# Optimization experiments

Hardware: AMD Instinct MI355X
Metric: run time of the kernel (lower is better)

The kernel has to match this reference:

```python
import jax, jax.numpy as jnp
import numpy as np
from jax import lax

B, S, H, D, NH, L, NC = 64, 512, 64, 128, 8, 4, 5
DT = 0.01

def _xavier(key, shape, gain=0.1):
    a = gain * np.sqrt(6.0 / (shape[0] + shape[1]))
    return jax.random.uniform(key, shape, jnp.float32, -a, a)

def setup_inputs():
    key = jax.random.key(0)
    ks = jax.random.split(key, 20)
    # strictly increasing positive times with spacing exactly dt -> one Euler step per interval
    times = (jnp.arange(S, dtype=jnp.float32) + 1.0) * DT
    feats = jax.random.uniform(ks[0], (B, S, 2), jnp.float32, 0.5, 5.0)
    time_series = jnp.concatenate([jnp.broadcast_to(times[None, :, None], (B, S, 1)), feats], axis=2)
    mask = jnp.ones((B, S), dtype=bool)
    noise = jax.random.normal(ks[1], (S - 1, B, H), jnp.float32)  # standard normal; scaled by sqrt(dt) inside
    n = lambda k, sh: 0.02 * jax.random.normal(k, sh, jnp.float32)
    return dict(
        time_series=time_series, mask=mask, noise=noise,
        dW1=_xavier(ks[2], (H + 1, 2 * H)), db1=jnp.zeros(2 * H, jnp.float32),
        dW2=_xavier(ks[3], (2 * H, H)), db2=jnp.zeros(H, jnp.float32),
        dW3=_xavier(ks[4], (H, H)), db3=jnp.zeros(H, jnp.float32),
        gW1=_xavier(ks[5], (H + 1, 2 * H)), gb1=jnp.zeros(2 * H, jnp.float32),
        gW2=_xavier(ks[6], (2 * H, H)), gb2=jnp.zeros(H, jnp.float32),
        min_diffusion=jnp.float32(0.05), max_drift=jnp.float32(1.0),
        in_W=n(ks[7], (H, D)), in_b=jnp.zeros(D, jnp.float32),
        Wq=n(ks[8], (L, D, D)), bq=jnp.zeros((L, D), jnp.float32),
        Wk=n(ks[9], (L, D, D)), bk=jnp.zeros((L, D), jnp.float32),
        Wv=n(ks[10], (L, D, D)), bv=jnp.zeros((L, D), jnp.float32),
        Wo=n(ks[11], (L, D, D)), bo=jnp.zeros((L, D), jnp.float32),
        ln1_s=jnp.ones((L, D), jnp.float32), ln1_b=jnp.zeros((L, D), jnp.float32),
        fW1=n(ks[12], (L, D, 4 * D)), fb1=jnp.zeros((L, 4 * D), jnp.float32),
        fW2=n(ks[13], (L, 4 * D, D)), fb2=jnp.zeros((L, D), jnp.float32),
        ln2_s=jnp.ones((L, D), jnp.float32), ln2_b=jnp.zeros((L, D), jnp.float32),
        cW1=n(ks[14], (D, D // 2)), cb1=jnp.zeros(D // 2, jnp.float32),
        cW2=n(ks[15], (D // 2, NC)), cb2=jnp.zeros(NC, jnp.float32),
    )

def _ln(x, s, b):
    m = x.mean(-1, keepdims=True)
    v = ((x - m) ** 2).mean(-1, keepdims=True)
    return (x - m) * lax.rsqrt(v + 1e-5) * s + b

def reference(time_series, mask, noise, dW1, db1, dW2, db2, dW3, db3,
              gW1, gb1, gW2, gb2, min_diffusion, max_drift,
              in_W, in_b, Wq, bq, Wk, bk, Wv, bv, Wo, bo,
              ln1_s, ln1_b, fW1, fb1, fW2, fb2, ln2_s, ln2_b,
              cW1, cb1, cW2, cb2):
    b, s = time_series.shape[:2]
    h = dW3.shape[1]
    nin = min(3, h)  # min(input_dim, hidden_channels)
    times = time_series[:, :, 0]

    # initial SDE state
    y0 = jnp.full((b, h), 0.1, time_series.dtype)
    y0 = y0.at[:, :nin].set(jnp.clip(time_series[:, 0, :nin], 0.01, 10.0))

    # per-interval left times, step sizes, Brownian increments (batch-shared time, element 0)
    ts0 = times[0]                        # (S,)
    t_left = ts0[:-1]                     # (S-1,)
    hstep = ts0[1:] - ts0[:-1]            # (S-1,)
    dW = noise * jnp.sqrt(hstep)[:, None, None]  # (S-1, B, H)

    def euler_step(y, inp):
        t, hh, dw = inp
        t_col = jnp.broadcast_to(jnp.reshape(t, (1, 1)), (y.shape[0], 1))
        ty = jnp.concatenate([y, t_col], axis=1)              # (B, H+1)
        # drift coeff net: Linear-Tanh-Linear-Tanh-Linear, clamped
        dc = jnp.tanh(ty @ dW1 + db1)
        dc = jnp.tanh(dc @ dW2 + db2)
        dc = dc @ dW3 + db3
        dc = jnp.clip(dc, -jnp.abs(max_drift), jnp.abs(max_drift))
        f = dc * y
        # diffusion coeff net: Linear-Tanh-Linear-Softplus + |min_diffusion|
        gc = jnp.tanh(ty @ gW1 + gb1)
        gc = jax.nn.softplus(gc @ gW2 + gb2) + jnp.abs(min_diffusion)
        g = gc * jnp.clip(y, -10.0, 10.0)
        y1 = jnp.clip(y + f * hh + g * dw, 0.01, 10.0)  # Euler-Maruyama + post-solve clamp
        return y1, y1

    _, traj = lax.scan(euler_step, y0, (t_left, hstep, dW))   # (S-1, B, H)
    sde_features = jnp.concatenate([y0[None], traj], axis=0).transpose(1, 0, 2)  # (B, S, H)
    mf = mask[..., None].astype(sde_features.dtype)
    sde_features = sde_features * mf

    # ContiFormer (standard post-LN transformer encoder over SDE features)
    x = sde_features @ in_W + in_b                            # (B, S, D)
    d = x.shape[-1]
    dh = d // NH
    scale = 1.0 / np.sqrt(dh)
    neg = jnp.asarray(-1e9, x.dtype)
    for l in range(Wq.shape[0]):
        q = (x @ Wq[l] + bq[l]).reshape(b, s, NH, dh)
        k = (x @ Wk[l] + bk[l]).reshape(b, s, NH, dh)
        v = (x @ Wv[l] + bv[l]).reshape(b, s, NH, dh)
        scores = jnp.einsum('bqhd,bkhd->bhqk', q, k) * scale
        scores = jnp.where(mask[:, None, None, :], scores, neg)
        attn = jax.nn.softmax(scores, axis=-1)
        o = jnp.einsum('bhqk,bkhd->bqhd', attn, v).reshape(b, s, d) @ Wo[l] + bo[l]
        x = _ln(x + o, ln1_s[l], ln1_b[l])
        ff = jax.nn.relu(x @ fW1[l] + fb1[l]) @ fW2[l] + fb2[l]
        x = _ln(x + ff, ln2_s[l], ln2_b[l])

    pooled = (x * mf).sum(1) / jnp.maximum(mf.sum(1), 1.0)    # masked mean pool (B, D)
    logits = jax.nn.relu(pooled @ cW1 + cb1) @ cW2 + cb2      # (B, NC)
    return (logits, sde_features)
```

## Files before the change

kernel.cpp:

```cpp
#include <hip/hip_runtime.h>
#include <hip/hip_bf16.h>
#include <math.h>

#define BB 64
#define SS 512
#define HH 64
#define DD 128
#define NHD 8
#define ROWS (BB*SS)

typedef unsigned short u16;
typedef __attribute__((ext_vector_type(8))) short bf16x8;
typedef __attribute__((ext_vector_type(4))) float f32x4;

__device__ __forceinline__ u16 f2b(float f) {
  union { float f; unsigned u; } x; x.f = f;
  unsigned r = x.u + 0x7fffu + ((x.u >> 16) & 1u);
  return (u16)(r >> 16);
}

__device__ __forceinline__ float b2f(u16 u) {
  return __uint_as_float(((unsigned)u) << 16);
}

__device__ __forceinline__ unsigned cvt_pk_bf16(float lo, float hi) {
  unsigned r;
  asm("v_cvt_pk_bf16_f32 %0, %1, %2" : "=v"(r) : "v"(lo), "v"(hi));
  return r;
}

__device__ __forceinline__ float fast_tanh(float x) {
  float ax = fminf(fabsf(x), 15.f);
  float e = __expf(2.f * ax);
  float r = 1.f - __fdividef(2.f, e + 1.f);
  return copysignf(r, x);
}

__device__ __forceinline__ void barrier_lds() {
  __builtin_amdgcn_s_waitcnt(0xC07F);
  __builtin_amdgcn_s_barrier();
}

__device__ __forceinline__ float dpp_xor1_add(float x) {
  int pi = __float_as_int(x);
  int po = __builtin_amdgcn_update_dpp(0, pi, 0xB1 ,
                                       0xF, 0xF, true);
  return x + __int_as_float(po);
}

template <int CTRL>
__device__ __forceinline__ float dpp_add(float x) {
  int po = __builtin_amdgcn_update_dpp(0, __float_as_int(x), CTRL, 0xF, 0xF, true);
  return x + __int_as_float(po);
}
__device__ __forceinline__ float red16(float x) {
  x = dpp_add<0xB1>(x);
  x = dpp_add<0x4E>(x);
  x = dpp_add<0x141>(x);
  x = dpp_add<0x140>(x);
  return x;
}

__global__ __attribute__((amdgpu_flat_work_group_size(512, 512)))
__attribute__((amdgpu_waves_per_eu(2, 2))) void sde_kernel(
    const float* __restrict__ ts, const float* __restrict__ noise,
    const float* __restrict__ dW1, const float* __restrict__ db1,
    const float* __restrict__ dW2, const float* __restrict__ db2,
    const float* __restrict__ dW3, const float* __restrict__ db3,
    const float* __restrict__ gW1, const float* __restrict__ gb1,
    const float* __restrict__ gW2, const float* __restrict__ gb2,
    const float* __restrict__ pmind, const float* __restrict__ pmaxd,
    float* __restrict__ out, u16* __restrict__ outB) {
  const int b = blockIdx.x, t = threadIdx.x;
  const int w = t >> 6, lane = t & 63;
  const int drift = (w < 4) ? 1 : 0;
  const int wseg = w & 3;

  __shared__ float y_s[8][64];
  __shared__ float h1seg[8][32];
  __shared__ float h2c[8][64];
  __shared__ float pd[2][4][64];
  __shared__ float pg[2][4][64];
  __shared__ float tl_s[512], hs_s[512], sq_s[512];

  const float mind = fabsf(pmind[0]);
  const float maxd = fabsf(pmaxd[0]);

  const int colA = wseg * 32 + (lane >> 1);
  const int hA = lane & 1;
  const float* W1 = drift ? dW1 : gW1;
  float wA[32];
#pragma unroll
  for (int k = 0; k < 32; k++) wA[k] = W1[(hA * 32 + k) * 128 + colA];
  const float wAt = W1[64 * 128 + colA];
  const float bA = (drift ? db1 : gb1)[colA];

  const float* W2 = drift ? dW2 : gW2;
  float wB[32];
#pragma unroll
  for (int k = 0; k < 32; k++) wB[k] = W2[(wseg * 32 + k) * 64 + lane];
  const float bBd = db2[lane], bBg = gb2[lane];

  float wC[64];
#pragma unroll
  for (int k = 0; k < 64; k++) wC[k] = dW3[k * 64 + lane];
  const float bC = db3[lane];

  tl_s[t & 511] = ts[(t & 511) * 3];
  __syncthreads();
  if (t < 511) {
    float hh = tl_s[t + 1] - tl_s[t];
    hs_s[t] = hh;
    sq_s[t] = sqrtf(hh);
  }

  float ymine = 0.1f;
  if (lane < 3) ymine = fminf(fmaxf(ts[b * 1536 + lane], 0.01f), 10.f);
  y_s[w][lane] = ymine;
  if (w == 0) out[(long)b * 32768 + lane] = ymine;
  if (w == 1) outB[((long)b * 512) * 64 + lane] = f2b(ymine);

  const long nofs = (long)b * 64 + lane;
  float nz0 = noise[nofs];
  float nz1 = noise[4096 + nofs];
  float nz2 = noise[2 * 4096 + nofs];
  float nz3 = noise[3 * 4096 + nofs];
  __syncthreads();

  for (int i = 0; i < 511; i++) {
    const int buf = i & 1;
    const float tl = tl_s[i];
    const float hh = hs_s[i];
    const float sq = sq_s[i];

    const float nz = nz0;
    nz0 = nz1; nz1 = nz2; nz2 = nz3;
    if (i + 4 < 511) nz3 = noise[(long)(i + 4) * 4096 + nofs];

    float a0 = 0.f, a1 = 0.f, a2 = 0.f, a3 = 0.f;
#pragma unroll
    for (int g = 0; g < 8; g++) {
      float4 yv = *(const float4*)&y_s[w][hA * 32 + g * 4];
      a0 += yv.x * wA[g * 4 + 0];
      a1 += yv.y * wA[g * 4 + 1];
      a2 += yv.z * wA[g * 4 + 2];
      a3 += yv.w * wA[g * 4 + 3];
    }
    float p1 = (a0 + a1) + (a2 + a3);
    p1 += hA ? (tl * wAt) : bA;
    p1 = dpp_xor1_add(p1);
    float h1v = fast_tanh(p1);
    if (hA == 0) h1seg[w][lane >> 1] = h1v;

    float c0 = 0.f, c1 = 0.f, c2 = 0.f, c3 = 0.f;
#pragma unroll
    for (int g = 0; g < 8; g++) {
      float4 hv = *(const float4*)&h1seg[w][g * 4];
      c0 += hv.x * wB[g * 4 + 0];
      c1 += hv.y * wB[g * 4 + 1];
      c2 += hv.z * wB[g * 4 + 2];
      c3 += hv.w * wB[g * 4 + 3];
    }
    float psum = (c0 + c1) + (c2 + c3);
    if (drift) pd[buf][wseg][lane] = psum;
    else       pg[buf][wseg][lane] = psum;

    barrier_lds();

    float sd = ((pd[buf][0][lane] + pd[buf][1][lane]) +
                (pd[buf][2][lane] + pd[buf][3][lane])) + bBd;
    float h2v = fast_tanh(sd);
    float sg = ((pg[buf][0][lane] + pg[buf][1][lane]) +
                (pg[buf][2][lane] + pg[buf][3][lane])) + bBg;
    float gc = fmaxf(sg, 0.f) + __logf(1.f + __expf(-fabsf(sg))) + mind;
    h2c[w][lane] = h2v;

    float d0 = 0.f, d1 = 0.f, d2 = 0.f, d3 = 0.f;
#pragma unroll
    for (int g = 0; g < 16; g++) {
      float4 hv = *(const float4*)&h2c[w][g * 4];
      d0 += hv.x * wC[g * 4 + 0];
      d1 += hv.y * wC[g * 4 + 1];
      d2 += hv.z * wC[g * 4 + 2];
      d3 += hv.w * wC[g * 4 + 3];
    }
    float dc = fminf(fmaxf((d0 + d1) + (d2 + d3) + bC, -maxd), maxd);

    float yo = ymine;
    float yn = yo + dc * yo * hh + gc * fminf(fmaxf(yo, -10.f), 10.f) * nz * sq;
    yn = fminf(fmaxf(yn, 0.01f), 10.f);
    y_s[w][lane] = yn;
    ymine = yn;
    if (w == 0) out[(long)b * 32768 + (i + 1) * 64 + lane] = yn;
    if (w == 1) outB[((long)b * 512 + i + 1) * 64 + lane] = f2b(yn);
  }
}

__global__ __launch_bounds__(256) void prep_weights(
    const float* __restrict__ in_W, const float* __restrict__ Wq,
    const float* __restrict__ Wk, const float* __restrict__ Wv,
    const float* __restrict__ Wo, const float* __restrict__ fW1,
    const float* __restrict__ fW2,
    u16* __restrict__ inWt, u16* __restrict__ qkvWt, u16* __restrict__ Wot,
    u16* __restrict__ fW1t, u16* __restrict__ fW2t) {
  const int z = blockIdx.z, layer = blockIdx.y, tile = blockIdx.x;
  const float* src; u16* dst; int R, C, nl;
  switch (z) {
    case 0: src = in_W; dst = inWt; R = 64; C = 128; nl = 1; break;
    case 1: src = Wq + layer * 16384; dst = qkvWt + layer * 49152; R = 128; C = 128; nl = 4; break;
    case 2: src = Wk + layer * 16384; dst = qkvWt + layer * 49152 + 16384; R = 128; C = 128; nl = 4; break;
    case 3: src = Wv + layer * 16384; dst = qkvWt + layer * 49152 + 32768; R = 128; C = 128; nl = 4; break;
    case 4: src = Wo + layer * 16384; dst = Wot + layer * 16384; R = 128; C = 128; nl = 4; break;
    case 5: src = fW1 + layer * 65536; dst = fW1t + layer * 65536; R = 128; C = 512; nl = 4; break;
    default: src = fW2 + layer * 65536; dst = fW2t + layer * 65536; R = 512; C = 128; nl = 4; break;
  }
  const int nt = (R / 32) * (C / 32);
  if (layer >= nl || tile >= nt) return;
  const int tpr = C / 32;
  const int r0 = (tile / tpr) * 32, c0 = (tile % tpr) * 32;
  __shared__ float tl[32][33];
  const int tx = threadIdx.x & 31, ty = threadIdx.x >> 5;
#pragma unroll
  for (int p = 0; p < 4; p++)
    tl[ty + 8 * p][tx] = src[(long)(r0 + ty + 8 * p) * C + c0 + tx];
  __syncthreads();
#pragma unroll
  for (int p = 0; p < 4; p++)
    dst[(long)(c0 + ty + 8 * p) * R + r0 + tx] = f2b(tl[tx][ty + 8 * p]);
}

__global__ __launch_bounds__(256) void mfma_gemm(
    const u16* __restrict__ A, const u16* __restrict__ Bt,
    const float* __restrict__ bias, u16* __restrict__ outB, int K, int N) {
  __shared__ u16 As[128 * 40];
  __shared__ u16 Bs[64 * 40];
  const int t = threadIdx.x;
  const int nb = blockIdx.x * 64;
  const long mb = (long)blockIdx.y * 128;
  const int lane = t & 63, wave = t >> 6;
  const int wm = (wave >> 1) * 64, wn = (wave & 1) * 32;
  const int fr = lane & 15, quad = lane >> 4;

  f32x4 zero = {0.f, 0.f, 0.f, 0.f};
  f32x4 acc[4][2];
#pragma unroll
  for (int mi = 0; mi < 4; mi++)
#pragma unroll
    for (int ni = 0; ni < 2; ni++) acc[mi][ni] = zero;

  for (int k0 = 0; k0 < K; k0 += 32) {
#pragma unroll
    for (int p = 0; p < 2; p++) {
      int idx = t + p * 256, row = idx >> 2, seg = idx & 3;
      int4 v = *(const int4*)&A[(mb + row) * K + k0 + seg * 8];
      *(int4*)&As[row * 40 + seg * 8] = v;
    }
    {
      int row = t >> 2, seg = t & 3;
      int4 v = *(const int4*)&Bt[(long)(nb + row) * K + k0 + seg * 8];
      *(int4*)&Bs[row * 40 + seg * 8] = v;
    }
    __syncthreads();
    bf16x8 af[4], bfr[2];
#pragma unroll
    for (int mi = 0; mi < 4; mi++)
      af[mi] = *(const bf16x8*)&As[(wm + mi * 16 + fr) * 40 + quad * 8];
#pragma unroll
    for (int ni = 0; ni < 2; ni++)
      bfr[ni] = *(const bf16x8*)&Bs[(wn + ni * 16 + fr) * 40 + quad * 8];
#pragma unroll
    for (int mi = 0; mi < 4; mi++)
#pragma unroll
      for (int ni = 0; ni < 2; ni++)
        acc[mi][ni] = __builtin_amdgcn_mfma_f32_16x16x32_bf16(
            af[mi], bfr[ni], acc[mi][ni], 0, 0, 0);
    __syncthreads();
  }

#pragma unroll
  for (int mi = 0; mi < 4; mi++)
#pragma unroll
    for (int ni = 0; ni < 2; ni++) {
      int col = nb + wn + ni * 16 + fr;
      float bv = bias[col];
#pragma unroll
      for (int r = 0; r < 4; r++) {
        long row = mb + wm + mi * 16 + quad * 4 + r;
        outB[row * N + col] = f2b(acc[mi][ni][r] + bv);
      }
    }
}

__global__ __launch_bounds__(512, 1) void layer_tail(
    const u16* __restrict__ ob, const u16* __restrict__ Wot,
    const float* __restrict__ bo, const float* __restrict__ ln1s,
    const float* __restrict__ ln1b, const u16* __restrict__ W1t,
    const float* __restrict__ fb1, const u16* __restrict__ W2t,
    const float* __restrict__ fb2, const float* __restrict__ ln2s,
    const float* __restrict__ ln2b, u16* __restrict__ xb) {
  __shared__ u16 As[64 * 136];
  __shared__ u16 Hs[64 * 520];
  __shared__ float s1[64][8], s2[64][8];
  __shared__ float mst[64][2];
  const int t = threadIdx.x;
  const long mb = (long)blockIdx.x * 64;
  const int w = t >> 6, lane = t & 63;
  const int fr = lane & 15, quad = lane >> 4;
  const int col = w * 16 + fr;
  const f32x4 z4 = {0.f, 0.f, 0.f, 0.f};

#pragma unroll
  for (int p = 0; p < 2; p++) {
    int c = t + p * 512;
    int row = c >> 4, sub = c & 15;
    *(int4*)&As[row * 136 + sub * 8] =
        *(const int4*)&ob[(mb + row) * DD + sub * 8];
  }
  __syncthreads();

  bf16x8 af[4][4];
#pragma unroll
  for (int m = 0; m < 4; m++)
#pragma unroll
    for (int c = 0; c < 4; c++)
      af[m][c] = *(const bf16x8*)&As[(m * 16 + fr) * 136 + c * 32 + quad * 8];

  f32x4 acc[4] = {z4, z4, z4, z4};
#pragma unroll
  for (int kc = 0; kc < 4; kc++) {
    bf16x8 bfr = *(const bf16x8*)&Wot[col * 128 + kc * 32 + quad * 8];
#pragma unroll
    for (int m = 0; m < 4; m++)
      acc[m] = __builtin_amdgcn_mfma_f32_16x16x32_bf16(af[m][kc], bfr,
                                                       acc[m], 0, 0, 0);
  }

  const float bov = bo[col], g1 = ln1s[col], be1 = ln1b[col];
  float vv[4][4];
#pragma unroll
  for (int m = 0; m < 4; m++)
#pragma unroll
    for (int r = 0; r < 4; r++) {
      int row = m * 16 + quad * 4 + r;
      float v = acc[m][r] + bov + b2f(xb[(mb + row) * DD + col]);
      vv[m][r] = v;
      float s = red16(v);
      float ss = red16(v * v);
      if (fr == 0) { s1[row][w] = s; s2[row][w] = ss; }
    }
  __syncthreads();
  {
    int row = lane;
    float4 a = *(const float4*)&s1[row][0];
    float4 bq4 = *(const float4*)&s1[row][4];
    float sumv = ((a.x + a.y) + (a.z + a.w)) +
                 ((bq4.x + bq4.y) + (bq4.z + bq4.w));
    float4 cq = *(const float4*)&s2[row][0];
    float4 dq = *(const float4*)&s2[row][4];
    float sumsq = ((cq.x + cq.y) + (cq.z + cq.w)) +
                  ((dq.x + dq.y) + (dq.z + dq.w));
    float mean = sumv * (1.f / 128.f);
    float var = sumsq * (1.f / 128.f) - mean * mean;
    mst[row][0] = mean;
    mst[row][1] = rsqrtf(var + 1e-5f);
  }
  __syncthreads();

  float xr[4][4];
#pragma unroll
  for (int m = 0; m < 4; m++)
#pragma unroll
    for (int r = 0; r < 4; r++) {
      int row = m * 16 + quad * 4 + r;
      float xv = (vv[m][r] - mst[row][0]) * mst[row][1] * g1 + be1;
      xr[m][r] = xv;
      As[row * 136 + col] = f2b(xv);
    }
  __syncthreads();

  bf16x8 af2[4][4];
#pragma unroll
  for (int m = 0; m < 4; m++)
#pragma unroll
    for (int c = 0; c < 4; c++)
      af2[m][c] = *(const bf16x8*)&As[(m * 16 + fr) * 136 + c * 32 + quad * 8];

#pragma unroll
  for (int nn = 0; nn < 4; nn++) {
    const int nt = w * 4 + nn;
    bf16x8 bfr[4];
#pragma unroll
    for (int c = 0; c < 4; c++)
      bfr[c] = *(const bf16x8*)&W1t[(nt * 16 + fr) * 128 + c * 32 + quad * 8];
    f32x4 a1[4] = {z4, z4, z4, z4};
#pragma unroll
    for (int c = 0; c < 4; c++)
#pragma unroll
      for (int m = 0; m < 4; m++)
        a1[m] = __builtin_amdgcn_mfma_f32_16x16x32_bf16(af2[m][c], bfr[c],
                                                        a1[m], 0, 0, 0);
    const float bv = fb1[nt * 16 + fr];
#pragma unroll
    for (int m = 0; m < 4; m++)
#pragma unroll
      for (int r = 0; r < 4; r++)
        Hs[(m * 16 + quad * 4 + r) * 520 + nt * 16 + fr] =
            f2b(fmaxf(a1[m][r] + bv, 0.f));
  }
  __syncthreads();

  f32x4 acc2[4] = {z4, z4, z4, z4};
#pragma unroll
  for (int kc = 0; kc < 16; kc++) {
    bf16x8 bfr2 = *(const bf16x8*)&W2t[col * 512 + kc * 32 + quad * 8];
    bf16x8 a2[4];
#pragma unroll
    for (int m = 0; m < 4; m++)
      a2[m] = *(const bf16x8*)&Hs[(m * 16 + fr) * 520 + kc * 32 + quad * 8];
#pragma unroll
    for (int m = 0; m < 4; m++)
      acc2[m] = __builtin_amdgcn_mfma_f32_16x16x32_bf16(a2[m], bfr2,
                                                        acc2[m], 0, 0, 0);
  }

  const float bv2 = fb2[col], g2 = ln2s[col], be2 = ln2b[col];
#pragma unroll
  for (int m = 0; m < 4; m++)
#pragma unroll
    for (int r = 0; r < 4; r++) {
      int row = m * 16 + quad * 4 + r;
      float v = acc2[m][r] + bv2 + xr[m][r];
      vv[m][r] = v;
      float s = red16(v);
      float ss = red16(v * v);
      if (fr == 0) { s1[row][w] = s; s2[row][w] = ss; }
    }
  __syncthreads();
  {
    int row = lane;
    float4 a = *(const float4*)&s1[row][0];
    float4 bq4 = *(const float4*)&s1[row][4];
    float sumv = ((a.x + a.y) + (a.z + a.w)) +
                 ((bq4.x + bq4.y) + (bq4.z + bq4.w));
    float4 cq = *(const float4*)&s2[row][0];
    float4 dq = *(const float4*)&s2[row][4];
    float sumsq = ((cq.x + cq.y) + (cq.z + cq.w)) +
                  ((dq.x + dq.y) + (dq.z + dq.w));
    float mean = sumv * (1.f / 128.f);
    float var = sumsq * (1.f / 128.f) - mean * mean;
    mst[row][0] = mean;
    mst[row][1] = rsqrtf(var + 1e-5f);
  }
  __syncthreads();

#pragma unroll
  for (int m = 0; m < 4; m++)
#pragma unroll
    for (int r = 0; r < 4; r++) {
      int row = m * 16 + quad * 4 + r;
      xb[(mb + row) * DD + col] =
          f2b((vv[m][r] - mst[row][0]) * mst[row][1] * g2 + be2);
    }
}

__global__ __launch_bounds__(256, 2) void qkv_attn(
    const u16* __restrict__ xb, const u16* __restrict__ qkvW,
    const float* __restrict__ bq, const float* __restrict__ bk,
    const float* __restrict__ bv, u16* __restrict__ Og) {
  const int bh = blockIdx.x;
  const int b = bh >> 3, h = bh & 7;
  __shared__ u16 Ks[512 * 24];
  __shared__ u16 Vt[16 * 520];
  __shared__ u16 Qs[512 * 24];
  const int t = threadIdx.x;
  const int w = t >> 6, lane = t & 63;
  const int fr = lane & 15, quad = lane >> 4;
  const long obase = ((long)b * SS) * DD + h * 16;
  const u16* xrow = xb + (long)b * SS * DD;

  const u16* Wq_h = qkvW + (h * 16) * 128;
  const u16* Wk_h = qkvW + 16384 + (h * 16) * 128;
  const u16* Wv_h = qkvW + 32768 + (h * 16) * 128;
  bf16x8 wqf[4], wkf[4], wvf[4];
#pragma unroll
  for (int c = 0; c < 4; c++) {
    wqf[c] = *(const bf16x8*)&Wq_h[fr * 128 + c * 32 + quad * 8];
    wkf[c] = *(const bf16x8*)&Wk_h[fr * 128 + c * 32 + quad * 8];
    wvf[c] = *(const bf16x8*)&Wv_h[fr * 128 + c * 32 + quad * 8];
  }
  const float bqv = bq[h * 16 + fr];
  const float bkv = bk[h * 16 + fr];
  const float bvv = bv[h * 16 + fr];
  const f32x4 z4 = {0.f, 0.f, 0.f, 0.f};
  const float qscale = 0.25f * 1.4426950408889634f;

  for (int tile = w; tile < 32; tile += 4) {
    const int t0 = tile * 16;
    bf16x8 af[4];
#pragma unroll
    for (int c = 0; c < 4; c++)
      af[c] = *(const bf16x8*)&xrow[(t0 + fr) * 128 + c * 32 + quad * 8];
    f32x4 qa = z4, ka = z4, va = z4;
#pragma unroll
    for (int c = 0; c < 4; c++) {
      qa = __builtin_amdgcn_mfma_f32_16x16x32_bf16(af[c], wqf[c], qa, 0, 0, 0);
      ka = __builtin_amdgcn_mfma_f32_16x16x32_bf16(af[c], wkf[c], ka, 0, 0, 0);
      va = __builtin_amdgcn_mfma_f32_16x16x32_bf16(af[c], wvf[c], va, 0, 0, 0);
    }
#pragma unroll
    for (int r = 0; r < 4; r++) {
      int row = t0 + quad * 4 + r;
      Qs[row * 24 + fr] = f2b((qa[r] + bqv) * qscale);
      Ks[row * 24 + fr] = f2b(ka[r] + bkv);
    }
    {
      const int t0q = t0 + quad * 4;
      const int r40 = t0q & 31;
      const int vbase = (t0q & ~31) + ((r40 & 12) << 1) + ((r40 & 16) >> 2);
      uint2 vvv;
      vvv.x = cvt_pk_bf16(va[0] + bvv, va[1] + bvv);
      vvv.y = cvt_pk_bf16(va[2] + bvv, va[3] + bvv);
      *(uint2*)&Vt[fr * 520 + vbase] = vvv;
    }
  }
  __syncthreads();

  for (int qt = w; qt < 32; qt += 4) {
    const int q0 = qt * 16;
    bf16x8 qf = {0, 0, 0, 0, 0, 0, 0, 0};
    if (quad < 2)
      qf = *(const bf16x8*)&Qs[(q0 + fr) * 24 + quad * 8];
    f32x4 oacc = {0.f, 0.f, 0.f, 0.f};
    float rsacc = 0.f;

    for (int kt = 0; kt < 16; kt++) {
      const int k0 = kt * 32;
      bf16x8 kf0 = {0, 0, 0, 0, 0, 0, 0, 0};
      bf16x8 kf1 = {0, 0, 0, 0, 0, 0, 0, 0};
      if (quad < 2) {
        kf0 = *(const bf16x8*)&Ks[(k0 + fr) * 24 + quad * 8];
        kf1 = *(const bf16x8*)&Ks[(k0 + 16 + fr) * 24 + quad * 8];
      }
      f32x4 slo = __builtin_amdgcn_mfma_f32_16x16x32_bf16(kf0, qf, z4, 0, 0, 0);
      f32x4 shi = __builtin_amdgcn_mfma_f32_16x16x32_bf16(kf1, qf, z4, 0, 0, 0);
      float p[8];
#pragma unroll
      for (int r = 0; r < 4; r++) {
        p[r] = __builtin_amdgcn_exp2f(slo[r]);
        p[4 + r] = __builtin_amdgcn_exp2f(shi[r]);
      }
      rsacc += ((p[0] + p[1]) + (p[2] + p[3])) +
               ((p[4] + p[5]) + (p[6] + p[7]));

      union { unsigned i[4]; bf16x8 v; } pu;
      pu.i[0] = cvt_pk_bf16(p[0], p[1]);
      pu.i[1] = cvt_pk_bf16(p[2], p[3]);
      pu.i[2] = cvt_pk_bf16(p[4], p[5]);
      pu.i[3] = cvt_pk_bf16(p[6], p[7]);
      bf16x8 vf = *(const bf16x8*)&Vt[fr * 520 + k0 + quad * 8];
      oacc = __builtin_amdgcn_mfma_f32_16x16x32_bf16(vf, pu.v, oacc, 0, 0, 0);
    }

    float lrun = rsacc;
    lrun += __shfl_xor(lrun, 16);
    lrun += __shfl_xor(lrun, 32);
    float inv = __fdividef(1.f, lrun);
    uint2 o;
    o.x = cvt_pk_bf16(oacc[0] * inv, oacc[1] * inv);
    o.y = cvt_pk_bf16(oacc[2] * inv, oacc[3] * inv);
    *(uint2*)&Og[obase + (long)(q0 + fr) * DD + quad * 4] = o;
  }
}

__global__ __launch_bounds__(512) void pool_kernel(const u16* __restrict__ X,
                                                   float* __restrict__ P) {
  const int b = blockIdx.x, t = threadIdx.x;
  const int c = t & 127, sg = t >> 7;
  __shared__ float red[4][128];
  float acc = 0.f;
  for (int s = sg; s < SS; s += 4)
    acc += b2f(X[((long)b * SS + s) * DD + c]);
  red[sg][c] = acc;
  __syncthreads();
  if (t < 128)
    P[b * DD + t] =
        (red[0][t] + red[1][t] + red[2][t] + red[3][t]) * (1.f / 512.f);
}

__global__ __launch_bounds__(64) void cls_kernel(
    const float* __restrict__ P, const float* __restrict__ W1,
    const float* __restrict__ b1, const float* __restrict__ W2,
    const float* __restrict__ b2, float* __restrict__ L) {
  const int b = blockIdx.x, t = threadIdx.x;
  __shared__ float sp[128];
  __shared__ float sh[64];
  sp[t] = P[b * DD + t];
  sp[t + 64] = P[b * DD + 64 + t];
  __syncthreads();
  float acc = b1[t];
  for (int k = 0; k < 128; k++) acc += sp[k] * W1[k * 64 + t];
  sh[t] = fmaxf(acc, 0.f);
  __syncthreads();
  if (t < 5) {
    float acc2 = b2[t];
    for (int k = 0; k < 64; k++) acc2 += sh[k] * W2[k * 5 + t];
    L[b * 5 + t] = acc2;
  }
}

extern "C" void kernel_launch(void* const* d_in, const int* in_sizes, int n_in,
                              void* d_out, int out_size, void* d_ws, size_t ws_size,
                              hipStream_t stream) {
  const float* ts    = (const float*)d_in[0];
  const float* noise = (const float*)d_in[2];
  const float* dW1   = (const float*)d_in[3];
  const float* db1   = (const float*)d_in[4];
  const float* dW2   = (const float*)d_in[5];
  const float* db2   = (const float*)d_in[6];
  const float* dW3   = (const float*)d_in[7];
  const float* db3   = (const float*)d_in[8];
  const float* gW1   = (const float*)d_in[9];
  const float* gb1   = (const float*)d_in[10];
  const float* gW2   = (const float*)d_in[11];
  const float* gb2   = (const float*)d_in[12];
  const float* mind  = (const float*)d_in[13];
  const float* maxd  = (const float*)d_in[14];
  const float* in_W  = (const float*)d_in[15];
  const float* in_b  = (const float*)d_in[16];
  const float* Wq    = (const float*)d_in[17];
  const float* bq    = (const float*)d_in[18];
  const float* Wk    = (const float*)d_in[19];
  const float* bk    = (const float*)d_in[20];
  const float* Wv    = (const float*)d_in[21];
  const float* bv    = (const float*)d_in[22];
  const float* Wo    = (const float*)d_in[23];
  const float* bo    = (const float*)d_in[24];
  const float* ln1s  = (const float*)d_in[25];
  const float* ln1b  = (const float*)d_in[26];
  const float* fW1   = (const float*)d_in[27];
  const float* fb1   = (const float*)d_in[28];
  const float* fW2   = (const float*)d_in[29];
  const float* fb2   = (const float*)d_in[30];
  const float* ln2s  = (const float*)d_in[31];
  const float* ln2b  = (const float*)d_in[32];
  const float* cW1   = (const float*)d_in[33];
  const float* cb1   = (const float*)d_in[34];
  const float* cW2   = (const float*)d_in[35];
  const float* cb2   = (const float*)d_in[36];

  float* logits = (float*)d_out;
  float* sde    = logits + BB * 5;

  char* W = (char*)d_ws;
  u16*  bxb    = (u16*)(W);
  u16*  bob    = (u16*)(W + (40u << 20));
  u16*  bsb    = (u16*)(W + (48u << 20));
  u16*  wts    = (u16*)(W + (52u << 20));
  float* bp    = (float*)(W + (54u << 20));

  u16* inWt  = wts;
  u16* qkvWt = inWt + 8192;
  u16* Wot   = qkvWt + 196608;
  u16* fW1t  = Wot + 65536;
  u16* fW2t  = fW1t + 262144;

  prep_weights<<<dim3(64, 4, 7), 256, 0, stream>>>(in_W, Wq, Wk, Wv, Wo, fW1, fW2,
                                                   inWt, qkvWt, Wot, fW1t, fW2t);

  sde_kernel<<<64, 512, 0, stream>>>(ts, noise, dW1, db1, dW2, db2, dW3, db3,
                                     gW1, gb1, gW2, gb2, mind, maxd, sde, bsb);

  mfma_gemm<<<dim3(2, 256), 256, 0, stream>>>(bsb, inWt, in_b, bxb, 64, 128);

  for (int l = 0; l < 4; l++) {
    qkv_attn<<<BB * NHD, 256, 0, stream>>>(bxb, qkvWt + l * 49152,
                                           bq + l * DD, bk + l * DD, bv + l * DD,
                                           bob);
    layer_tail<<<512, 512, 0, stream>>>(bob, Wot + l * 16384, bo + l * DD,
                                        ln1s + l * DD, ln1b + l * DD,
                                        fW1t + l * 65536, fb1 + l * 512,
                                        fW2t + l * 65536, fb2 + l * DD,
                                        ln2s + l * DD, ln2b + l * DD, bxb);
  }

  pool_kernel<<<BB, 512, 0, stream>>>(bxb, bp);
  cls_kernel<<<BB, 64, 0, stream>>>(bp, cW1, cb1, cW2, cb2, logits);
}
```

Before: 1.049 ms.

## Cut LDS and register use in layer_tail and qkv_attn to raise occupancy

```diff
diff --git a/kernel.cpp b/kernel.cpp
--- a/kernel.cpp
+++ b/kernel.cpp
@@ -39,6 +39,10 @@
 __device__ __forceinline__ void barrier_lds() {
   __builtin_amdgcn_s_waitcnt(0xC07F);
   __builtin_amdgcn_s_barrier();
+}
+
+__device__ __forceinline__ void wait_lds() {
+  __builtin_amdgcn_s_waitcnt(0xC07F);
 }
 
 __device__ __forceinline__ float dpp_xor1_add(float x) {
@@ -291,7 +295,7 @@
     }
 }
 
-__global__ __launch_bounds__(512, 1) void layer_tail(
+__global__ __launch_bounds__(512, 4) void layer_tail(
     const u16* __restrict__ ob, const u16* __restrict__ Wot,
     const float* __restrict__ bo, const float* __restrict__ ln1s,
     const float* __restrict__ ln1b, const u16* __restrict__ W1t,
@@ -299,7 +303,7 @@
     const float* __restrict__ fb2, const float* __restrict__ ln2s,
     const float* __restrict__ ln2b, u16* __restrict__ xb) {
   __shared__ u16 As[64 * 136];
-  __shared__ u16 Hs[64 * 520];
+  __shared__ u16 Hs[64 * 264];
   __shared__ float s1[64][8], s2[64][8];
   __shared__ float mst[64][2];
   const int t = threadIdx.x;
@@ -318,21 +322,15 @@
   }
   __syncthreads();
 
-  bf16x8 af[4][4];
-#pragma unroll
-  for (int m = 0; m < 4; m++)
-#pragma unroll
-    for (int c = 0; c < 4; c++)
-      af[m][c] = *(const bf16x8*)&As[(m * 16 + fr) * 136 + c * 32 + quad * 8];
-
   f32x4 acc[4] = {z4, z4, z4, z4};
 #pragma unroll
   for (int kc = 0; kc < 4; kc++) {
     bf16x8 bfr = *(const bf16x8*)&Wot[col * 128 + kc * 32 + quad * 8];
 #pragma unroll
-    for (int m = 0; m < 4; m++)
-      acc[m] = __builtin_amdgcn_mfma_f32_16x16x32_bf16(af[m][kc], bfr,
-                                                       acc[m], 0, 0, 0);
+    for (int m = 0; m < 4; m++) {
+      bf16x8 a = *(const bf16x8*)&As[(m * 16 + fr) * 136 + kc * 32 + quad * 8];
+      acc[m] = __builtin_amdgcn_mfma_f32_16x16x32_bf16(a, bfr, acc[m], 0, 0, 0);
+    }
   }
 
   const float bov = bo[col], g1 = ln1s[col], be1 = ln1b[col];
@@ -378,49 +376,48 @@
     }
   __syncthreads();
 
-  bf16x8 af2[4][4];
-#pragma unroll
-  for (int m = 0; m < 4; m++)
-#pragma unroll
-    for (int c = 0; c < 4; c++)
-      af2[m][c] = *(const bf16x8*)&As[(m * 16 + fr) * 136 + c * 32 + quad * 8];
-
-#pragma unroll
-  for (int nn = 0; nn < 4; nn++) {
-    const int nt = w * 4 + nn;
-    bf16x8 bfr[4];
-#pragma unroll
-    for (int c = 0; c < 4; c++)
-      bfr[c] = *(const bf16x8*)&W1t[(nt * 16 + fr) * 128 + c * 32 + quad * 8];
-    f32x4 a1[4] = {z4, z4, z4, z4};
-#pragma unroll
-    for (int c = 0; c < 4; c++)
+  f32x4 acc2[4] = {z4, z4, z4, z4};
+#pragma unroll
+  for (int c = 0; c < 2; c++) {
+    if (c) __syncthreads();
+#pragma unroll
+    for (int nn = 0; nn < 2; nn++) {
+      const int ntl = w * 2 + nn;
+      const int ntg = c * 16 + ntl;
+      f32x4 a1[4] = {z4, z4, z4, z4};
+#pragma unroll
+      for (int cc = 0; cc < 4; cc++) {
+        bf16x8 bfr =
+            *(const bf16x8*)&W1t[(ntg * 16 + fr) * 128 + cc * 32 + quad * 8];
+#pragma unroll
+        for (int m = 0; m < 4; m++) {
+          bf16x8 a =
+              *(const bf16x8*)&As[(m * 16 + fr) * 136 + cc * 32 + quad * 8];
+          a1[m] =
+              __builtin_amdgcn_mfma_f32_16x16x32_bf16(a, bfr, a1[m], 0, 0, 0);
+        }
+      }
+      const float bv = fb1[ntg * 16 + fr];
 #pragma unroll
       for (int m = 0; m < 4; m++)
-        a1[m] = __builtin_amdgcn_mfma_f32_16x16x32_bf16(af2[m][c], bfr[c],
-                                                        a1[m], 0, 0, 0);
-    const float bv = fb1[nt * 16 + fr];
-#pragma unroll
-    for (int m = 0; m < 4; m++)
-#pragma unroll
-      for (int r = 0; r < 4; r++)
-        Hs[(m * 16 + quad * 4 + r) * 520 + nt * 16 + fr] =
-            f2b(fmaxf(a1[m][r] + bv, 0.f));
-  }
-  __syncthreads();
-
-  f32x4 acc2[4] = {z4, z4, z4, z4};
-#pragma unroll
-  for (int kc = 0; kc < 16; kc++) {
-    bf16x8 bfr2 = *(const bf16x8*)&W2t[col * 512 + kc * 32 + quad * 8];
-    bf16x8 a2[4];
-#pragma unroll
-    for (int m = 0; m < 4; m++)
-      a2[m] = *(const bf16x8*)&Hs[(m * 16 + fr) * 520 + kc * 32 + quad * 8];
-#pragma unroll
-    for (int m = 0; m < 4; m++)
-      acc2[m] = __builtin_amdgcn_mfma_f32_16x16x32_bf16(a2[m], bfr2,
-                                                        acc2[m], 0, 0, 0);
+#pragma unroll
+        for (int r = 0; r < 4; r++)
+          Hs[(m * 16 + quad * 4 + r) * 264 + ntl * 16 + fr] =
+              f2b(fmaxf(a1[m][r] + bv, 0.f));
+    }
+    __syncthreads();
+#pragma unroll
+    for (int kc = 0; kc < 8; kc++) {
+      bf16x8 bfr2 =
+          *(const bf16x8*)&W2t[col * 512 + c * 256 + kc * 32 + quad * 8];
+#pragma unroll
+      for (int m = 0; m < 4; m++) {
+        bf16x8 a2 =
+            *(const bf16x8*)&Hs[(m * 16 + fr) * 264 + kc * 32 + quad * 8];
+        acc2[m] = __builtin_amdgcn_mfma_f32_16x16x32_bf16(a2, bfr2,
+                                                          acc2[m], 0, 0, 0);
+      }
+    }
   }
 
   const float bv2 = fb2[col], g2 = ln2s[col], be2 = ln2b[col];
@@ -463,7 +460,7 @@
     }
 }
 
-__global__ __launch_bounds__(256, 2) void qkv_attn(
+__global__ __launch_bounds__(256, 3) void qkv_attn(
     const u16* __restrict__ xb, const u16* __restrict__ qkvW,
     const float* __restrict__ bq, const float* __restrict__ bk,
     const float* __restrict__ bv, u16* __restrict__ Og) {
@@ -471,7 +468,7 @@
   const int b = bh >> 3, h = bh & 7;
   __shared__ u16 Ks[512 * 24];
   __shared__ u16 Vt[16 * 520];
-  __shared__ u16 Qs[512 * 24];
+  __shared__ u16 Qsc[4][16 * 24];
   const int t = threadIdx.x;
   const int w = t >> 6, lane = t & 63;
   const int fr = lane & 15, quad = lane >> 4;
@@ -494,8 +491,10 @@
   const f32x4 z4 = {0.f, 0.f, 0.f, 0.f};
   const float qscale = 0.25f * 1.4426950408889634f;
 
-  for (int tile = w; tile < 32; tile += 4) {
-    const int t0 = tile * 16;
+  bf16x8 qreg[8];
+#pragma unroll
+  for (int ti = 0; ti < 8; ti++) {
+    const int t0 = (w + ti * 4) * 16;
     bf16x8 af[4];
 #pragma unroll
     for (int c = 0; c < 4; c++)
@@ -510,8 +509,8 @@
 #pragma unroll
     for (int r = 0; r < 4; r++) {
       int row = t0 + quad * 4 + r;
-      Qs[row * 24 + fr] = f2b((qa[r] + bqv) * qscale);
       Ks[row * 24 + fr] = f2b(ka[r] + bkv);
+      Qsc[w][(quad * 4 + r) * 24 + fr] = f2b((qa[r] + bqv) * qscale);
     }
     {
       const int t0q = t0 + quad * 4;
@@ -522,14 +521,18 @@
       vvv.y = cvt_pk_bf16(va[2] + bvv, va[3] + bvv);
       *(uint2*)&Vt[fr * 520 + vbase] = vvv;
     }
-  }
-  __syncthreads();
-
-  for (int qt = w; qt < 32; qt += 4) {
-    const int q0 = qt * 16;
+    wait_lds();
     bf16x8 qf = {0, 0, 0, 0, 0, 0, 0, 0};
     if (quad < 2)
-      qf = *(const bf16x8*)&Qs[(q0 + fr) * 24 + quad * 8];
+      qf = *(const bf16x8*)&Qsc[w][fr * 24 + quad * 8];
+    qreg[ti] = qf;
+  }
+  __syncthreads();
+
+#pragma unroll
+  for (int ti = 0; ti < 8; ti++) {
+    const int q0 = (w + ti * 4) * 16;
+    const bf16x8 qf = qreg[ti];
     f32x4 oacc = {0.f, 0.f, 0.f, 0.f};
     float rsacc = 0.f;
 
```

Result: slower. 1.156 ms (+10.2%).
